# Optimization experiments

Measured on AMD Instinct MI355X. Metric: run time of the kernel, lower is better.

The kernel has to match this reference:

```python
import jax, jax.numpy as jnp
import numpy as np

N, E = 50000, 300000
NI, EI, H, OUT, L = 16, 8, 64, 3, 3  # node/edge input widths, hidden, output, conv_depth


def setup_inputs() -> dict:
    key = jax.random.key(0)
    ks = iter(jax.random.split(key, 64))
    def rn(shape, scale=0.05):
        return jax.random.normal(next(ks), shape, dtype=jnp.float32) * scale
    inp = {}
    inp["nodes"] = jax.random.normal(next(ks), (N, NI), dtype=jnp.float32)
    inp["edges"] = jax.random.normal(next(ks), (E, EI), dtype=jnp.float32)
    inp["edge_idx"] = jax.random.randint(next(ks), (E, 2), 0, N, dtype=jnp.int32)
    def mlp_params(prefix, din, lead=None):
        s = () if lead is None else (lead,)
        inp[prefix + "_W1"] = rn(s + (din, H))
        inp[prefix + "_b1"] = jnp.zeros(s + (H,), jnp.float32)
        inp[prefix + "_W2"] = rn(s + (H, H))
        inp[prefix + "_b2"] = jnp.zeros(s + (H,), jnp.float32)
        inp[prefix + "_g"] = jnp.ones(s + (H,), jnp.float32)
        inp[prefix + "_be"] = jnp.zeros(s + (H,), jnp.float32)
    mlp_params("ne", NI)            # node encoder
    mlp_params("ee", EI)            # edge encoder
    mlp_params("nm", 2 * H, lead=L)  # node messengers (stacked over conv_depth)
    mlp_params("em", 3 * H, lead=L)  # edge messengers
    inp["dec_W1"] = rn((H, H)); inp["dec_b1"] = jnp.zeros((H,), jnp.float32)
    inp["dec_W2"] = rn((H, OUT)); inp["dec_b2"] = jnp.zeros((OUT,), jnp.float32)
    return inp


def _lrelu(x):
    return jnp.where(x >= 0, x, 0.05 * x)


def _ln(x, g, b):
    m = jnp.mean(x, axis=-1, keepdims=True)
    v = jnp.mean((x - m) ** 2, axis=-1, keepdims=True)
    return (x - m) * jax.lax.rsqrt(v + 1e-5) * g + b


def _mlp(x, W1, b1, W2, b2, g, b):
    h = _lrelu(x @ W1 + b1)
    h = _lrelu(h @ W2 + b2)
    return _ln(h, g, b)


def reference(nodes, edges, edge_idx,
              ne_W1, ne_b1, ne_W2, ne_b2, ne_g, ne_be,
              ee_W1, ee_b1, ee_W2, ee_b2, ee_g, ee_be,
              nm_W1, nm_b1, nm_W2, nm_b2, nm_g, nm_be,
              em_W1, em_b1, em_W2, em_b2, em_g, em_be,
              dec_W1, dec_b1, dec_W2, dec_b2):
    n = _mlp(nodes, ne_W1, ne_b1, ne_W2, ne_b2, ne_g, ne_be)   # [N, H]
    e = _mlp(edges, ee_W1, ee_b1, ee_W2, ee_b2, ee_g, ee_be)   # [E, H]
    s, r = edge_idx[:, 0], edge_idx[:, 1]
    for i in range(L):
        e = e + _mlp(jnp.concatenate([e, n[s], n[r]], axis=1),
                     em_W1[i], em_b1[i], em_W2[i], em_b2[i], em_g[i], em_be[i])
        aggr = jax.ops.segment_sum(e, s, num_segments=n.shape[0])  # scatter_add onto senders
        n = n + _mlp(jnp.concatenate([n, aggr], axis=1),
                     nm_W1[i], nm_b1[i], nm_W2[i], nm_b2[i], nm_g[i], nm_be[i])
    h = _lrelu(n @ dec_W1 + dec_b1)
    return h @ dec_W2 + dec_b2  # [N, OUT]
```

## Files before the change

### kernel.cpp

```cpp
#include <hip/hip_runtime.h>

constexpr int BT = 256;

typedef __attribute__((ext_vector_type(8))) short short8v;
typedef __attribute__((ext_vector_type(4))) short short4v;
typedef __attribute__((ext_vector_type(4))) float f32x4;

__device__ __forceinline__ float lrelu(float x) { return x >= 0.f ? x : 0.05f * x; }

__device__ __forceinline__ unsigned short bf16_rne(float x) {
    unsigned u = __float_as_uint(x);
    u += 0x7FFFu + ((u >> 16) & 1u);
    return (unsigned short)(u >> 16);
}
__device__ __forceinline__ float bf16_to_f(unsigned short h) {
    return __uint_as_float(((unsigned)h) << 16);
}
__device__ __forceinline__ void split2(float x, unsigned short& hi, unsigned short& lo) {
    hi = bf16_rne(x);
    lo = bf16_rne(x - bf16_to_f(hi));
}


__device__ __forceinline__ void stageA64(const float* __restrict__ src, int row0, int nrows,
                                         short* __restrict__ A)
{
    for (int q = threadIdx.x; q < 1024; q += 256) {
        const int row = q >> 4;
        const int k0 = (q & 15) << 2;
        const int grow = row0 + row;
        float4 x = (grow < nrows) ? *reinterpret_cast<const float4*>(src + (long long)grow * 64 + k0)
                                  : make_float4(0.f, 0.f, 0.f, 0.f);
        unsigned short h0,h1,h2,h3,l0,l1,l2,l3;
        split2(x.x, h0, l0); split2(x.y, h1, l1); split2(x.z, h2, l2); split2(x.w, h3, l3);
        const int off = row * 64 + ((((k0 >> 3) ^ (row & 7))) << 3) + (k0 & 7);
        short4v hv; hv[0]=(short)h0; hv[1]=(short)h1; hv[2]=(short)h2; hv[3]=(short)h3;
        short4v lv; lv[0]=(short)l0; lv[1]=(short)l1; lv[2]=(short)l2; lv[3]=(short)l3;
        *reinterpret_cast<short4v*>(A + off) = hv;
        *reinterpret_cast<short4v*>(A + 4096 + off) = lv;
    }
}

__device__ __forceinline__ void gemm64(const short* __restrict__ A, const short* __restrict__ wf,
                                       int row, int g, int lane, f32x4* __restrict__ acc)
{
    #pragma unroll
    for (int s = 0; s < 2; ++s) {
        const int k8 = s * 4 + g;
        const int aoff = row * 64 + ((k8 ^ (row & 7)) << 3);
        const short8v a_hi = *reinterpret_cast<const short8v*>(A + aoff);
        const short8v a_lo = *reinterpret_cast<const short8v*>(A + 4096 + aoff);
        #pragma unroll
        for (int t = 0; t < 4; ++t) {
            const short8v b_hi = *reinterpret_cast<const short8v*>(wf + ((s*4+t)*2+0)*512 + lane*8);
            const short8v b_lo = *reinterpret_cast<const short8v*>(wf + ((s*4+t)*2+1)*512 + lane*8);
            acc[t] = __builtin_amdgcn_mfma_f32_16x16x32_bf16(a_hi, b_hi, acc[t], 0, 0, 0);
            acc[t] = __builtin_amdgcn_mfma_f32_16x16x32_bf16(a_lo, b_hi, acc[t], 0, 0, 0);
            acc[t] = __builtin_amdgcn_mfma_f32_16x16x32_bf16(a_hi, b_lo, acc[t], 0, 0, 0);
        }
    }
}

__global__ void k_prepw(const float* __restrict__ emW1, const float* __restrict__ emW2,
                        const float* __restrict__ nmW1, const float* __restrict__ nmW2,
                        const float* __restrict__ eeW2, const float* __restrict__ neW2,
                        const float* __restrict__ decW1,
                        short* __restrict__ wf)
{
    const int cid = blockIdx.x;
    const float* src;
    if (cid < 21) {
        const int layer = cid / 7, j = cid % 7;
        src =
            j == 0 ? emW1 + (size_t)layer * 12288 :
            j == 1 ? emW1 + (size_t)layer * 12288 + 4096 :
            j == 2 ? emW1 + (size_t)layer * 12288 + 8192 :
            j == 3 ? emW2 + (size_t)layer * 4096 :
            j == 4 ? nmW1 + (size_t)layer * 8192 :
            j == 5 ? nmW1 + (size_t)layer * 8192 + 4096 :
                     nmW2 + (size_t)layer * 4096;
    } else {
        src = (cid == 21) ? eeW2 : (cid == 22) ? neW2 : decW1;
    }
    short* dst = wf + (size_t)cid * 8192;
    for (int fr = threadIdx.x; fr < 1024; fr += 256) {
        const int lane = fr & 63;
        const int stp = fr >> 6;
        const int p = stp & 1;
        const int st = stp >> 1;
        const int s = st >> 2, t = st & 3;
        const int col = ((lane & 15) << 2) + t;
        const int k0 = s * 32 + (lane >> 4) * 8;
        short8v o;
        #pragma unroll
        for (int i = 0; i < 8; ++i) {
            const float w = src[(k0 + i) * 64 + col];
            const unsigned short hi = bf16_rne(w);
            o[i] = (short)(p ? bf16_rne(w - bf16_to_f(hi)) : hi);
        }
        *reinterpret_cast<short8v*>(dst + fr * 8) = o;
    }
}

template<int DIN, bool PERM>
__global__ __launch_bounds__(256) void k_enc_mf(
    const float* __restrict__ x, const int* __restrict__ csr,
    const float* __restrict__ W1, const float* __restrict__ b1,
    const short* __restrict__ wfW2, const float* __restrict__ b2,
    const float* __restrict__ gam, const float* __restrict__ bet,
    float* __restrict__ out, int nrows)
{
    __shared__ short Hf[8192];
    const int row0 = blockIdx.x * 64;
    const int lane = threadIdx.x & 63;
    const int wm = threadIdx.x >> 6;
    const int g = lane >> 4, c = lane & 15;
    const int c4 = c << 2;
    const int rowA = wm * 16 + c;

    long long orig[4];
    #pragma unroll
    for (int r = 0; r < 4; ++r) {
        const int grow = row0 + wm * 16 + g * 4 + r;
        orig[r] = (grow < nrows) ? (long long)(PERM ? csr[grow] : grow) : -1;
    }

    const f32x4 z4 = {0.f, 0.f, 0.f, 0.f};
    f32x4 acc[4];
    #pragma unroll
    for (int t = 0; t < 4; ++t) acc[t] = z4;

    #pragma unroll
    for (int kq = 0; kq < DIN / 4; ++kq) {
        float xv[4][4];
        #pragma unroll
        for (int r = 0; r < 4; ++r) {
            float4 t4 = make_float4(0.f, 0.f, 0.f, 0.f);
            if (orig[r] >= 0)
                t4 = *reinterpret_cast<const float4*>(x + orig[r] * DIN + kq * 4);
            xv[r][0] = t4.x; xv[r][1] = t4.y; xv[r][2] = t4.z; xv[r][3] = t4.w;
        }
        #pragma unroll
        for (int i = 0; i < 4; ++i) {
            const int k = kq * 4 + i;
            const float4 w4 = *reinterpret_cast<const float4*>(W1 + k * 64 + c4);
            const float wv[4] = {w4.x, w4.y, w4.z, w4.w};
            #pragma unroll
            for (int t = 0; t < 4; ++t)
                #pragma unroll
                for (int r = 0; r < 4; ++r)
                    acc[t][r] = fmaf(xv[r][i], wv[t], acc[t][r]);
        }
    }

    const float4 b1q = *reinterpret_cast<const float4*>(b1 + c4);
    const float b1a[4] = {b1q.x, b1q.y, b1q.z, b1q.w};
    #pragma unroll
    for (int r = 0; r < 4; ++r) {
        const int rl = wm * 16 + g * 4 + r;
        const int off = rl * 64 + (((c4 >> 3) ^ (rl & 7)) << 3) + (c4 & 7);
        short4v hv, lv;
        #pragma unroll
        for (int t = 0; t < 4; ++t) {
            const float h = lrelu(acc[t][r] + b1a[t]);
            unsigned short hi, lo; split2(h, hi, lo);
            hv[t] = (short)hi; lv[t] = (short)lo;
        }
        *reinterpret_cast<short4v*>(Hf + off) = hv;
        *reinterpret_cast<short4v*>(Hf + 4096 + off) = lv;
    }

    f32x4 acc2[4];
    #pragma unroll
    for (int t = 0; t < 4; ++t) acc2[t] = z4;
    gemm64(Hf, wfW2, rowA, g, lane, acc2);

    const float4 b2q = *reinterpret_cast<const float4*>(b2 + c4);
    const float b2a[4] = {b2q.x, b2q.y, b2q.z, b2q.w};
    #pragma unroll
    for (int t = 0; t < 4; ++t) {
        #pragma unroll
        for (int r = 0; r < 4; ++r) acc2[t][r] = lrelu(acc2[t][r] + b2a[t]);
    }
    const float4 gq = *reinterpret_cast<const float4*>(gam + c4);
    const float4 bq = *reinterpret_cast<const float4*>(bet + c4);
    const float gv[4] = {gq.x, gq.y, gq.z, gq.w};
    const float bv[4] = {bq.x, bq.y, bq.z, bq.w};
    #pragma unroll
    for (int r = 0; r < 4; ++r) {
        float s = acc2[0][r] + acc2[1][r] + acc2[2][r] + acc2[3][r];
        s += __shfl_xor(s, 1); s += __shfl_xor(s, 2); s += __shfl_xor(s, 4); s += __shfl_xor(s, 8);
        const float mu = s * 0.015625f;
        float q = 0.f;
        #pragma unroll
        for (int t = 0; t < 4; ++t) { const float d = acc2[t][r] - mu; q = fmaf(d, d, q); }
        q += __shfl_xor(q, 1); q += __shfl_xor(q, 2); q += __shfl_xor(q, 4); q += __shfl_xor(q, 8);
        const float rs = rsqrtf(q * 0.015625f + 1e-5f);
        const int grow = row0 + wm * 16 + g * 4 + r;
        if (grow < nrows) {
            float4 o;
            o.x = (acc2[0][r] - mu) * rs * gv[0] + bv[0];
            o.y = (acc2[1][r] - mu) * rs * gv[1] + bv[1];
            o.z = (acc2[2][r] - mu) * rs * gv[2] + bv[2];
            o.w = (acc2[3][r] - mu) * rs * gv[3] + bv[3];
            *reinterpret_cast<float4*>(out + (long long)grow * 64 + c4) = o;
        }
    }
}

__global__ __launch_bounds__(256) void k_uv_mf(
    const float* __restrict__ n, const short* __restrict__ wfB, const short* __restrict__ wfC,
    float* __restrict__ u, float* __restrict__ v, int N)
{
    __shared__ short Ab[8192];
    const int row0 = blockIdx.x * 64;
    stageA64(n, row0, N, Ab);
    __syncthreads();
    const int lane = threadIdx.x & 63;
    const int wm = threadIdx.x >> 6;
    const int g = lane >> 4, c = lane & 15;
    const int c4 = c << 2;
    const int rowA = wm * 16 + c;
    const f32x4 z4 = {0.f, 0.f, 0.f, 0.f};
    f32x4 acc[4];
    #pragma unroll
    for (int t = 0; t < 4; ++t) acc[t] = z4;
    gemm64(Ab, wfB, rowA, g, lane, acc);
    #pragma unroll
    for (int r = 0; r < 4; ++r) {
        const int grow = row0 + wm * 16 + g * 4 + r;
        if (grow < N) {
            float4 o; o.x = acc[0][r]; o.y = acc[1][r]; o.z = acc[2][r]; o.w = acc[3][r];
            *reinterpret_cast<float4*>(u + (long long)grow * 64 + c4) = o;
        }
    }
    #pragma unroll
    for (int t = 0; t < 4; ++t) acc[t] = z4;
    gemm64(Ab, wfC, rowA, g, lane, acc);
    #pragma unroll
    for (int r = 0; r < 4; ++r) {
        const int grow = row0 + wm * 16 + g * 4 + r;
        if (grow < N) {
            float4 o; o.x = acc[0][r]; o.y = acc[1][r]; o.z = acc[2][r]; o.w = acc[3][r];
            *reinterpret_cast<float4*>(v + (long long)grow * 64 + c4) = o;
        }
    }
}

__global__ __launch_bounds__(256, 4) void k_edge_mf(
    float* __restrict__ e, const int* __restrict__ sp, const int* __restrict__ rp,
    const float* __restrict__ u, const float* __restrict__ v,
    const short* __restrict__ wfA, const short* __restrict__ wfW2,
    const float* __restrict__ b1, const float* __restrict__ b2,
    const float* __restrict__ gam, const float* __restrict__ bet, int E)
{
    __shared__ short Ab[8192];
    const int row0 = blockIdx.x * 64;
    const int lane = threadIdx.x & 63;
    const int wm = threadIdx.x >> 6;
    const int g = lane >> 4, c = lane & 15;
    const int c4 = c << 2;
    const int rowA = wm * 16 + c;

    int sidx[4], ridx[4];
    #pragma unroll
    for (int r = 0; r < 4; ++r) {
        const int grow = row0 + wm * 16 + g * 4 + r;
        if (grow < E) { sidx[r] = sp[grow]; ridx[r] = rp[grow]; }
        else          { sidx[r] = 0; ridx[r] = 0; }
    }
    float4 uu[4], vv[4];
    #pragma unroll
    for (int r = 0; r < 4; ++r) {
        uu[r] = *reinterpret_cast<const float4*>(u + (long long)sidx[r] * 64 + c4);
        vv[r] = *reinterpret_cast<const float4*>(v + (long long)ridx[r] * 64 + c4);
    }

    stageA64(e, row0, E, Ab);
    __syncthreads();

    const f32x4 z4 = {0.f, 0.f, 0.f, 0.f};
    f32x4 acc[4];
    #pragma unroll
    for (int t = 0; t < 4; ++t) acc[t] = z4;
    gemm64(Ab, wfA, rowA, g, lane, acc);

    const float4 b1q = *reinterpret_cast<const float4*>(b1 + c4);
    #pragma unroll
    for (int r = 0; r < 4; ++r) {
        acc[0][r] += b1q.x + uu[r].x + vv[r].x;
        acc[1][r] += b1q.y + uu[r].y + vv[r].y;
        acc[2][r] += b1q.z + uu[r].z + vv[r].z;
        acc[3][r] += b1q.w + uu[r].w + vv[r].w;
    }
    short4v eh[4], el[4];
    #pragma unroll
    for (int r = 0; r < 4; ++r) {
        const int rl = wm * 16 + g * 4 + r;
        const int off = rl * 64 + (((c4 >> 3) ^ (rl & 7)) << 3) + (c4 & 7);
        eh[r] = *reinterpret_cast<const short4v*>(Ab + off);
        el[r] = *reinterpret_cast<const short4v*>(Ab + 4096 + off);
        short4v hv, lv;
        #pragma unroll
        for (int t = 0; t < 4; ++t) {
            const float h = lrelu(acc[t][r]);
            unsigned short hi, lo; split2(h, hi, lo);
            hv[t] = (short)hi; lv[t] = (short)lo;
        }
        *reinterpret_cast<short4v*>(Ab + off) = hv;
        *reinterpret_cast<short4v*>(Ab + 4096 + off) = lv;
    }
    f32x4 acc2[4];
    #pragma unroll
    for (int t = 0; t < 4; ++t) acc2[t] = z4;
    gemm64(Ab, wfW2, rowA, g, lane, acc2);

    const float4 b2q = *reinterpret_cast<const float4*>(b2 + c4);
    const float b2a[4] = {b2q.x, b2q.y, b2q.z, b2q.w};
    #pragma unroll
    for (int t = 0; t < 4; ++t) {
        #pragma unroll
        for (int r = 0; r < 4; ++r) acc2[t][r] = lrelu(acc2[t][r] + b2a[t]);
    }
    const float4 gq = *reinterpret_cast<const float4*>(gam + c4);
    const float4 bq = *reinterpret_cast<const float4*>(bet + c4);
    const float gv[4] = {gq.x, gq.y, gq.z, gq.w};
    const float bv[4] = {bq.x, bq.y, bq.z, bq.w};
    #pragma unroll
    for (int r = 0; r < 4; ++r) {
        float s = acc2[0][r] + acc2[1][r] + acc2[2][r] + acc2[3][r];
        s += __shfl_xor(s, 1); s += __shfl_xor(s, 2); s += __shfl_xor(s, 4); s += __shfl_xor(s, 8);
        const float mu = s * 0.015625f;
        float q = 0.f;
        #pragma unroll
        for (int t = 0; t < 4; ++t) { const float d = acc2[t][r] - mu; q = fmaf(d, d, q); }
        q += __shfl_xor(q, 1); q += __shfl_xor(q, 2); q += __shfl_xor(q, 4); q += __shfl_xor(q, 8);
        const float rs = rsqrtf(q * 0.015625f + 1e-5f);
        const int grow = row0 + wm * 16 + g * 4 + r;
        if (grow < E) {
            float4 o;
            o.x = (acc2[0][r] - mu) * rs * gv[0] + bv[0] + bf16_to_f((unsigned short)eh[r][0]) + bf16_to_f((unsigned short)el[r][0]);
            o.y = (acc2[1][r] - mu) * rs * gv[1] + bv[1] + bf16_to_f((unsigned short)eh[r][1]) + bf16_to_f((unsigned short)el[r][1]);
            o.z = (acc2[2][r] - mu) * rs * gv[2] + bv[2] + bf16_to_f((unsigned short)eh[r][2]) + bf16_to_f((unsigned short)el[r][2]);
            o.w = (acc2[3][r] - mu) * rs * gv[3] + bv[3] + bf16_to_f((unsigned short)eh[r][3]) + bf16_to_f((unsigned short)el[r][3]);
            *reinterpret_cast<float4*>(e + (long long)grow * 64 + c4) = o;
        }
    }
}

__global__ __launch_bounds__(256) void k_node_mf(
    float* __restrict__ n, const float* __restrict__ aggr,
    const short* __restrict__ wfW1a, const short* __restrict__ wfW1b, const short* __restrict__ wfW2,
    const float* __restrict__ b1, const float* __restrict__ b2,
    const float* __restrict__ gam, const float* __restrict__ bet, int N)
{
    __shared__ short An[8192];
    __shared__ short Aa[8192];
    const int row0 = blockIdx.x * 64;
    stageA64(n, row0, N, An);
    stageA64(aggr, row0, N, Aa);
    __syncthreads();
    const int lane = threadIdx.x & 63;
    const int wm = threadIdx.x >> 6;
    const int g = lane >> 4, c = lane & 15;
    const int c4 = c << 2;
    const int rowA = wm * 16 + c;
    const f32x4 z4 = {0.f, 0.f, 0.f, 0.f};
    f32x4 acc[4];
    #pragma unroll
    for (int t = 0; t < 4; ++t) acc[t] = z4;
    gemm64(An, wfW1a, rowA, g, lane, acc);
    gemm64(Aa, wfW1b, rowA, g, lane, acc);

    const float4 b1q = *reinterpret_cast<const float4*>(b1 + c4);
    const float b1a[4] = {b1q.x, b1q.y, b1q.z, b1q.w};
    #pragma unroll
    for (int r = 0; r < 4; ++r) {
        const int rl = wm * 16 + g * 4 + r;
        const int off = rl * 64 + (((c4 >> 3) ^ (rl & 7)) << 3) + (c4 & 7);
        short4v hv, lv;
        #pragma unroll
        for (int t = 0; t < 4; ++t) {
            const float h = lrelu(acc[t][r] + b1a[t]);
            unsigned short hi, lo; split2(h, hi, lo);
            hv[t] = (short)hi; lv[t] = (short)lo;
        }
        *reinterpret_cast<short4v*>(Aa + off) = hv;
        *reinterpret_cast<short4v*>(Aa + 4096 + off) = lv;
    }
    f32x4 acc2[4];
    #pragma unroll
    for (int t = 0; t < 4; ++t) acc2[t] = z4;
    gemm64(Aa, wfW2, rowA, g, lane, acc2);

    const float4 b2q = *reinterpret_cast<const float4*>(b2 + c4);
    const float b2a[4] = {b2q.x, b2q.y, b2q.z, b2q.w};
    #pragma unroll
    for (int t = 0; t < 4; ++t) {
        #pragma unroll
        for (int r = 0; r < 4; ++r) acc2[t][r] = lrelu(acc2[t][r] + b2a[t]);
    }
    const float4 gq = *reinterpret_cast<const float4*>(gam + c4);
    const float4 bq = *reinterpret_cast<const float4*>(bet + c4);
    const float gv[4] = {gq.x, gq.y, gq.z, gq.w};
    const float bv[4] = {bq.x, bq.y, bq.z, bq.w};
    #pragma unroll
    for (int r = 0; r < 4; ++r) {
        float s = acc2[0][r] + acc2[1][r] + acc2[2][r] + acc2[3][r];
        s += __shfl_xor(s, 1); s += __shfl_xor(s, 2); s += __shfl_xor(s, 4); s += __shfl_xor(s, 8);
        const float mu = s * 0.015625f;
        float q = 0.f;
        #pragma unroll
        for (int t = 0; t < 4; ++t) { const float d = acc2[t][r] - mu; q = fmaf(d, d, q); }
        q += __shfl_xor(q, 1); q += __shfl_xor(q, 2); q += __shfl_xor(q, 4); q += __shfl_xor(q, 8);
        const float rs = rsqrtf(q * 0.015625f + 1e-5f);
        const int rl = wm * 16 + g * 4 + r;
        const int grow = row0 + rl;
        if (grow < N) {
            const int off = rl * 64 + (((c4 >> 3) ^ (rl & 7)) << 3) + (c4 & 7);
            const short4v nh = *reinterpret_cast<const short4v*>(An + off);
            const short4v nl = *reinterpret_cast<const short4v*>(An + 4096 + off);
            float4 o;
            o.x = (acc2[0][r] - mu) * rs * gv[0] + bv[0] + bf16_to_f((unsigned short)nh[0]) + bf16_to_f((unsigned short)nl[0]);
            o.y = (acc2[1][r] - mu) * rs * gv[1] + bv[1] + bf16_to_f((unsigned short)nh[1]) + bf16_to_f((unsigned short)nl[1]);
            o.z = (acc2[2][r] - mu) * rs * gv[2] + bv[2] + bf16_to_f((unsigned short)nh[2]) + bf16_to_f((unsigned short)nl[2]);
            o.w = (acc2[3][r] - mu) * rs * gv[3] + bv[3] + bf16_to_f((unsigned short)nh[3]) + bf16_to_f((unsigned short)nl[3]);
            *reinterpret_cast<float4*>(n + (long long)grow * 64 + c4) = o;
        }
    }
}

__global__ __launch_bounds__(256) void k_dec_mf(
    const float* __restrict__ n, const short* __restrict__ wfW1, const float* __restrict__ b1,
    const float* __restrict__ W2, const float* __restrict__ b2,
    float* __restrict__ out, int N)
{
    __shared__ short An[8192];
    float* hrow = reinterpret_cast<float*>(An);
    const int row0 = blockIdx.x * 64;
    stageA64(n, row0, N, An);
    __syncthreads();
    const int lane = threadIdx.x & 63;
    const int wm = threadIdx.x >> 6;
    const int g = lane >> 4, c = lane & 15;
    const int c4 = c << 2;
    const int rowA = wm * 16 + c;
    const f32x4 z4 = {0.f, 0.f, 0.f, 0.f};
    f32x4 acc[4];
    #pragma unroll
    for (int t = 0; t < 4; ++t) acc[t] = z4;
    gemm64(An, wfW1, rowA, g, lane, acc);
    const float4 b1q = *reinterpret_cast<const float4*>(b1 + c4);
    const float b1a[4] = {b1q.x, b1q.y, b1q.z, b1q.w};
    __syncthreads();
    #pragma unroll
    for (int t = 0; t < 4; ++t) {
        const int col = c4 + t;
        #pragma unroll
        for (int r = 0; r < 4; ++r) {
            const int rl = wm * 16 + g * 4 + r;
            hrow[rl * 64 + (col ^ (rl & 31))] = lrelu(acc[t][r] + b1a[t]);
        }
    }
    __syncthreads();
    const int row = threadIdx.x >> 2, o = threadIdx.x & 3;
    if (o < 3 && row0 + row < N) {
        float s = b2[o];
        #pragma unroll 8
        for (int k = 0; k < 64; ++k)
            s = fmaf(hrow[row * 64 + (k ^ (row & 31))], W2[k * 3 + o], s);
        out[(long long)(row0 + row) * 3 + o] = s;
    }
}

__global__ void k_hist(const int* __restrict__ eidx, int* __restrict__ cnt, int E)
{
    int i = blockIdx.x * 256 + threadIdx.x;
    if (i < E) atomicAdd(&cnt[eidx[2 * i]], 1);
}

__global__ void k_scan1(const int* __restrict__ cnt, int* __restrict__ starts,
                        int* __restrict__ bsum, int n)
{
    __shared__ int sh[256];
    const int tid = threadIdx.x;
    const int i = blockIdx.x * 256 + tid;
    const int val = (i < n) ? cnt[i] : 0;
    sh[tid] = val; __syncthreads();
    for (int off = 1; off < 256; off <<= 1) {
        int t = (tid >= off) ? sh[tid - off] : 0;
        __syncthreads();
        sh[tid] += t;
        __syncthreads();
    }
    if (i < n) starts[i] = sh[tid] - val;
    if (tid == 255) bsum[blockIdx.x] = sh[255];
}

__global__ void k_scan2(int* __restrict__ bsum, int nb)
{
    __shared__ int sh[256];
    const int tid = threadIdx.x;
    const int val = (tid < nb) ? bsum[tid] : 0;
    sh[tid] = val; __syncthreads();
    for (int off = 1; off < 256; off <<= 1) {
        int t = (tid >= off) ? sh[tid - off] : 0;
        __syncthreads();
        sh[tid] += t;
        __syncthreads();
    }
    if (tid < nb) bsum[tid] = sh[tid] - val;
}

__global__ void k_scan3(int* __restrict__ starts, const int* __restrict__ bsum, int n)
{
    int i = blockIdx.x * 256 + threadIdx.x;
    if (i < n) starts[i] += bsum[blockIdx.x];
}

__global__ void k_scatter(const int* __restrict__ eidx, const int* __restrict__ starts,
                          int* __restrict__ cursor, int* __restrict__ csr,
                          int* __restrict__ sp, int* __restrict__ rp, int E)
{
    int i = blockIdx.x * 256 + threadIdx.x;
    if (i < E) {
        const int s = eidx[2 * i];
        const int p = atomicAdd(&cursor[s], 1);
        const int q = starts[s] + p;
        csr[q] = i;
        sp[q] = s;
        rp[q] = eidx[2 * i + 1];
    }
}

__global__ __launch_bounds__(256) void k_aggr(
    const float* __restrict__ e, const int* __restrict__ starts, const int* __restrict__ cnt,
    float* __restrict__ aggr, int N)
{
    const int node = blockIdx.x * 4 + (threadIdx.x >> 6);
    if (node >= N) return;
    const int j = threadIdx.x & 63;
    const int st = starts[node], en = st + cnt[node];
    float a = 0.f;
    for (int t = st; t < en; ++t)
        a += e[(long long)t * 64 + j];
    aggr[(long long)node * 64 + j] = a;
}

extern "C" void kernel_launch(void* const* d_in, const int* in_sizes, int n_in,
                              void* d_out, int out_size, void* d_ws, size_t ws_size,
                              hipStream_t stream)
{
    (void)in_sizes; (void)n_in; (void)out_size; (void)ws_size;
    constexpr int N = 50000, E = 300000, L = 3;

    const float* nodes = (const float*)d_in[0];
    const float* edges = (const float*)d_in[1];
    const int*   eidx  = (const int*)d_in[2];
    const float* neW1 = (const float*)d_in[3];
    const float* neb1 = (const float*)d_in[4];
    const float* neW2 = (const float*)d_in[5];
    const float* neb2 = (const float*)d_in[6];
    const float* neg  = (const float*)d_in[7];
    const float* nebe = (const float*)d_in[8];
    const float* eeW1 = (const float*)d_in[9];
    const float* eeb1 = (const float*)d_in[10];
    const float* eeW2 = (const float*)d_in[11];
    const float* eeb2 = (const float*)d_in[12];
    const float* eeg  = (const float*)d_in[13];
    const float* eebe = (const float*)d_in[14];
    const float* nmW1 = (const float*)d_in[15];
    const float* nmb1 = (const float*)d_in[16];
    const float* nmW2 = (const float*)d_in[17];
    const float* nmb2 = (const float*)d_in[18];
    const float* nmg  = (const float*)d_in[19];
    const float* nmbe = (const float*)d_in[20];
    const float* emW1 = (const float*)d_in[21];
    const float* emb1 = (const float*)d_in[22];
    const float* emW2 = (const float*)d_in[23];
    const float* emb2 = (const float*)d_in[24];
    const float* emg  = (const float*)d_in[25];
    const float* embe = (const float*)d_in[26];
    const float* decW1 = (const float*)d_in[27];
    const float* decb1 = (const float*)d_in[28];
    const float* decW2 = (const float*)d_in[29];
    const float* decb2 = (const float*)d_in[30];

    float* n   = (float*)d_ws;
    float* u   = n + (size_t)N * 64;
    float* v   = u + (size_t)N * 64;
    float* e   = v + (size_t)N * 64;
    int* cnt    = (int*)(e + (size_t)E * 64);
    int* starts = cnt + N;
    int* csr    = starts + N;
    int* bsum   = csr + E;
    int* cursor = bsum + 256;
    int* sp     = cursor + N;
    int* rp     = sp + E;
    short* wf   = (short*)(rp + E);

    const int nbN = (N + BT - 1) / BT;
    const int nbE = (E + BT - 1) / BT;
    const int nbN64 = (N + 63) / 64;
    const int nbE64 = (E + 63) / 64;

    const short* wfEE  = wf + (size_t)21 * 8192;
    const short* wfNE  = wf + (size_t)22 * 8192;
    const short* wfDec = wf + (size_t)23 * 8192;

    k_prepw<<<24, 256, 0, stream>>>(emW1, emW2, nmW1, nmW2, eeW2, neW2, decW1, wf);
    hipMemsetAsync(cnt, 0, (size_t)N * sizeof(int), stream);
    hipMemsetAsync(cursor, 0, (size_t)N * sizeof(int), stream);
    k_hist<<<nbE, 256, 0, stream>>>(eidx, cnt, E);
    k_scan1<<<nbN, 256, 0, stream>>>(cnt, starts, bsum, N);
    k_scan2<<<1, 256, 0, stream>>>(bsum, nbN);
    k_scan3<<<nbN, 256, 0, stream>>>(starts, bsum, N);
    k_scatter<<<nbE, 256, 0, stream>>>(eidx, starts, cursor, csr, sp, rp, E);

    k_enc_mf<16, false><<<nbN64, 256, 0, stream>>>(nodes, nullptr, neW1, neb1, wfNE,
                                                   neb2, neg, nebe, n, N);
    k_enc_mf<8, true><<<nbE64, 256, 0, stream>>>(edges, csr, eeW1, eeb1, wfEE,
                                                 eeb2, eeg, eebe, e, E);

    for (int i = 0; i < L; ++i) {
        const short* wl = wf + (size_t)i * 7 * 8192;
        k_uv_mf<<<nbN64, 256, 0, stream>>>(n, wl + 8192, wl + 2 * 8192, u, v, N);
        k_edge_mf<<<nbE64, 256, 0, stream>>>(e, sp, rp, u, v, wl, wl + 3 * 8192,
                                             emb1 + i * 64, emb2 + i * 64,
                                             emg + i * 64, embe + i * 64, E);
        k_aggr<<<(N + 3) / 4, 256, 0, stream>>>(e, starts, cnt, u, N);
        k_node_mf<<<nbN64, 256, 0, stream>>>(n, u, wl + 4 * 8192, wl + 5 * 8192, wl + 6 * 8192,
                                             nmb1 + i * 64, nmb2 + i * 64,
                                             nmg + i * 64, nmbe + i * 64, N);
    }
    k_dec_mf<<<nbN64, 256, 0, stream>>>(n, wfDec, decb1, decW2, decb2, (float*)d_out, N);
}
```

Baseline: 472.8 us.

## Fuse u/v projection and segment aggregation into node kernels, use wave-local staging

Removes the separate k_uv_mf and k_aggr kernels. The next layer's u/v projections are now computed inside the node-encoder and node-update kernels, and the CSR segment sum is computed inside the node kernel. Shared-memory staging is made per-wave, so block-wide __syncthreads become wave barriers, and occupancy hints are raised. The decoder's second layer now uses shuffle reductions instead of an LDS round trip. This cuts launches and global round trips for u, v and aggr, but the node kernel now does a serial, load-imbalanced gather per wave over 16 nodes.

New measurement: 489.8 us. 3.6% more time.

```diff
diff --git a/kernel.cpp b/kernel.cpp
--- a/kernel.cpp
+++ b/kernel.cpp
@@ -1,6 +1,4 @@
 #include <hip/hip_runtime.h>
-
-constexpr int BT = 256;
 
 typedef __attribute__((ext_vector_type(8))) short short8v;
 typedef __attribute__((ext_vector_type(4))) short short4v;
@@ -22,18 +20,20 @@
 }
 
 
-__device__ __forceinline__ void stageA64(const float* __restrict__ src, int row0, int nrows,
-                                         short* __restrict__ A)
-{
-    for (int q = threadIdx.x; q < 1024; q += 256) {
-        const int row = q >> 4;
+__device__ __forceinline__ void stageW(const float* __restrict__ src, int row0, int nrows,
+                                       short* __restrict__ A, int wm, int lane)
+{
+    #pragma unroll
+    for (int it = 0; it < 4; ++it) {
+        const int q = it * 64 + lane;
+        const int rl = wm * 16 + (q >> 4);
         const int k0 = (q & 15) << 2;
-        const int grow = row0 + row;
+        const int grow = row0 + rl;
         float4 x = (grow < nrows) ? *reinterpret_cast<const float4*>(src + (long long)grow * 64 + k0)
                                   : make_float4(0.f, 0.f, 0.f, 0.f);
         unsigned short h0,h1,h2,h3,l0,l1,l2,l3;
         split2(x.x, h0, l0); split2(x.y, h1, l1); split2(x.z, h2, l2); split2(x.w, h3, l3);
-        const int off = row * 64 + ((((k0 >> 3) ^ (row & 7))) << 3) + (k0 & 7);
+        const int off = rl * 64 + ((((k0 >> 3) ^ (rl & 7))) << 3) + (k0 & 7);
         short4v hv; hv[0]=(short)h0; hv[1]=(short)h1; hv[2]=(short)h2; hv[3]=(short)h3;
         short4v lv; lv[0]=(short)l0; lv[1]=(short)l1; lv[2]=(short)l2; lv[3]=(short)l3;
         *reinterpret_cast<short4v*>(A + off) = hv;
@@ -58,6 +58,22 @@
             acc[t] = __builtin_amdgcn_mfma_f32_16x16x32_bf16(a_lo, b_hi, acc[t], 0, 0, 0);
             acc[t] = __builtin_amdgcn_mfma_f32_16x16x32_bf16(a_hi, b_lo, acc[t], 0, 0, 0);
         }
+    }
+}
+
+__device__ __forceinline__ void repackW(short* __restrict__ A, const float4* __restrict__ q,
+                                        int wm, int g, int c4)
+{
+    #pragma unroll
+    for (int r = 0; r < 4; ++r) {
+        const int rl = wm * 16 + g * 4 + r;
+        const int off = rl * 64 + (((c4 >> 3) ^ (rl & 7)) << 3) + (c4 & 7);
+        unsigned short h0,h1,h2,h3,l0,l1,l2,l3;
+        split2(q[r].x, h0, l0); split2(q[r].y, h1, l1); split2(q[r].z, h2, l2); split2(q[r].w, h3, l3);
+        short4v hv; hv[0]=(short)h0; hv[1]=(short)h1; hv[2]=(short)h2; hv[3]=(short)h3;
+        short4v lv; lv[0]=(short)l0; lv[1]=(short)l1; lv[2]=(short)l2; lv[3]=(short)l3;
+        *reinterpret_cast<short4v*>(A + off) = hv;
+        *reinterpret_cast<short4v*>(A + 4096 + off) = lv;
     }
 }
 
@@ -102,13 +118,15 @@
     }
 }
 
-template<int DIN, bool PERM>
-__global__ __launch_bounds__(256) void k_enc_mf(
+template<int DIN, bool PERM, bool MAKEUV>
+__global__ __launch_bounds__(256, 4) void k_enc_mf(
     const float* __restrict__ x, const int* __restrict__ csr,
     const float* __restrict__ W1, const float* __restrict__ b1,
     const short* __restrict__ wfW2, const float* __restrict__ b2,
     const float* __restrict__ gam, const float* __restrict__ bet,
-    float* __restrict__ out, int nrows)
+    float* __restrict__ out,
+    const short* __restrict__ wfB, const short* __restrict__ wfC,
+    float* __restrict__ u, float* __restrict__ v, int nrows)
 {
     __shared__ short Hf[8192];
     const int row0 = blockIdx.x * 64;
@@ -154,21 +172,16 @@
     }
 
     const float4 b1q = *reinterpret_cast<const float4*>(b1 + c4);
-    const float b1a[4] = {b1q.x, b1q.y, b1q.z, b1q.w};
-    #pragma unroll
-    for (int r = 0; r < 4; ++r) {
-        const int rl = wm * 16 + g * 4 + r;
-        const int off = rl * 64 + (((c4 >> 3) ^ (rl & 7)) << 3) + (c4 & 7);
-        short4v hv, lv;
-        #pragma unroll
-        for (int t = 0; t < 4; ++t) {
-            const float h = lrelu(acc[t][r] + b1a[t]);
-            unsigned short hi, lo; split2(h, hi, lo);
-            hv[t] = (short)hi; lv[t] = (short)lo;
-        }
-        *reinterpret_cast<short4v*>(Hf + off) = hv;
-        *reinterpret_cast<short4v*>(Hf + 4096 + off) = lv;
-    }
+    float4 hq[4];
+    #pragma unroll
+    for (int r = 0; r < 4; ++r) {
+        hq[r].x = lrelu(acc[0][r] + b1q.x);
+        hq[r].y = lrelu(acc[1][r] + b1q.y);
+        hq[r].z = lrelu(acc[2][r] + b1q.z);
+        hq[r].w = lrelu(acc[3][r] + b1q.w);
+    }
+    repackW(Hf, hq, wm, g, c4);
+    __builtin_amdgcn_wave_barrier();
 
     f32x4 acc2[4];
     #pragma unroll
@@ -184,8 +197,7 @@
     }
     const float4 gq = *reinterpret_cast<const float4*>(gam + c4);
     const float4 bq = *reinterpret_cast<const float4*>(bet + c4);
-    const float gv[4] = {gq.x, gq.y, gq.z, gq.w};
-    const float bv[4] = {bq.x, bq.y, bq.z, bq.w};
+    float4 nq[4];
     #pragma unroll
     for (int r = 0; r < 4; ++r) {
         float s = acc2[0][r] + acc2[1][r] + acc2[2][r] + acc2[3][r];
@@ -196,58 +208,44 @@
         for (int t = 0; t < 4; ++t) { const float d = acc2[t][r] - mu; q = fmaf(d, d, q); }
         q += __shfl_xor(q, 1); q += __shfl_xor(q, 2); q += __shfl_xor(q, 4); q += __shfl_xor(q, 8);
         const float rs = rsqrtf(q * 0.015625f + 1e-5f);
+        nq[r].x = (acc2[0][r] - mu) * rs * gq.x + bq.x;
+        nq[r].y = (acc2[1][r] - mu) * rs * gq.y + bq.y;
+        nq[r].z = (acc2[2][r] - mu) * rs * gq.z + bq.z;
+        nq[r].w = (acc2[3][r] - mu) * rs * gq.w + bq.w;
         const int grow = row0 + wm * 16 + g * 4 + r;
-        if (grow < nrows) {
-            float4 o;
-            o.x = (acc2[0][r] - mu) * rs * gv[0] + bv[0];
-            o.y = (acc2[1][r] - mu) * rs * gv[1] + bv[1];
-            o.z = (acc2[2][r] - mu) * rs * gv[2] + bv[2];
-            o.w = (acc2[3][r] - mu) * rs * gv[3] + bv[3];
-            *reinterpret_cast<float4*>(out + (long long)grow * 64 + c4) = o;
-        }
-    }
-}
-
-__global__ __launch_bounds__(256) void k_uv_mf(
-    const float* __restrict__ n, const short* __restrict__ wfB, const short* __restrict__ wfC,
-    float* __restrict__ u, float* __restrict__ v, int N)
-{
-    __shared__ short Ab[8192];
-    const int row0 = blockIdx.x * 64;
-    stageA64(n, row0, N, Ab);
-    __syncthreads();
-    const int lane = threadIdx.x & 63;
-    const int wm = threadIdx.x >> 6;
-    const int g = lane >> 4, c = lane & 15;
-    const int c4 = c << 2;
-    const int rowA = wm * 16 + c;
-    const f32x4 z4 = {0.f, 0.f, 0.f, 0.f};
-    f32x4 acc[4];
-    #pragma unroll
-    for (int t = 0; t < 4; ++t) acc[t] = z4;
-    gemm64(Ab, wfB, rowA, g, lane, acc);
-    #pragma unroll
-    for (int r = 0; r < 4; ++r) {
-        const int grow = row0 + wm * 16 + g * 4 + r;
-        if (grow < N) {
-            float4 o; o.x = acc[0][r]; o.y = acc[1][r]; o.z = acc[2][r]; o.w = acc[3][r];
-            *reinterpret_cast<float4*>(u + (long long)grow * 64 + c4) = o;
-        }
-    }
-    #pragma unroll
-    for (int t = 0; t < 4; ++t) acc[t] = z4;
-    gemm64(Ab, wfC, rowA, g, lane, acc);
-    #pragma unroll
-    for (int r = 0; r < 4; ++r) {
-        const int grow = row0 + wm * 16 + g * 4 + r;
-        if (grow < N) {
-            float4 o; o.x = acc[0][r]; o.y = acc[1][r]; o.z = acc[2][r]; o.w = acc[3][r];
-            *reinterpret_cast<float4*>(v + (long long)grow * 64 + c4) = o;
-        }
-    }
-}
-
-__global__ __launch_bounds__(256, 4) void k_edge_mf(
+        if (grow < nrows)
+            *reinterpret_cast<float4*>(out + (long long)grow * 64 + c4) = nq[r];
+    }
+
+    if (MAKEUV) {
+        repackW(Hf, nq, wm, g, c4);
+        __builtin_amdgcn_wave_barrier();
+        #pragma unroll
+        for (int t = 0; t < 4; ++t) acc2[t] = z4;
+        gemm64(Hf, wfB, rowA, g, lane, acc2);
+        #pragma unroll
+        for (int r = 0; r < 4; ++r) {
+            const int grow = row0 + wm * 16 + g * 4 + r;
+            if (grow < nrows) {
+                float4 o; o.x = acc2[0][r]; o.y = acc2[1][r]; o.z = acc2[2][r]; o.w = acc2[3][r];
+                *reinterpret_cast<float4*>(u + (long long)grow * 64 + c4) = o;
+            }
+        }
+        #pragma unroll
+        for (int t = 0; t < 4; ++t) acc2[t] = z4;
+        gemm64(Hf, wfC, rowA, g, lane, acc2);
+        #pragma unroll
+        for (int r = 0; r < 4; ++r) {
+            const int grow = row0 + wm * 16 + g * 4 + r;
+            if (grow < nrows) {
+                float4 o; o.x = acc2[0][r]; o.y = acc2[1][r]; o.z = acc2[2][r]; o.w = acc2[3][r];
+                *reinterpret_cast<float4*>(v + (long long)grow * 64 + c4) = o;
+            }
+        }
+    }
+}
+
+__global__ __launch_bounds__(256, 6) void k_edge_mf(
     float* __restrict__ e, const int* __restrict__ sp, const int* __restrict__ rp,
     const float* __restrict__ u, const float* __restrict__ v,
     const short* __restrict__ wfA, const short* __restrict__ wfW2,
@@ -269,6 +267,8 @@
         if (grow < E) { sidx[r] = sp[grow]; ridx[r] = rp[grow]; }
         else          { sidx[r] = 0; ridx[r] = 0; }
     }
+    stageW(e, row0, E, Ab, wm, lane);
+    __builtin_amdgcn_wave_barrier();
     float4 uu[4], vv[4];
     #pragma unroll
     for (int r = 0; r < 4; ++r) {
@@ -276,9 +276,6 @@
         vv[r] = *reinterpret_cast<const float4*>(v + (long long)ridx[r] * 64 + c4);
     }
 
-    stageA64(e, row0, E, Ab);
-    __syncthreads();
-
     const f32x4 z4 = {0.f, 0.f, 0.f, 0.f};
     f32x4 acc[4];
     #pragma unroll
@@ -286,12 +283,13 @@
     gemm64(Ab, wfA, rowA, g, lane, acc);
 
     const float4 b1q = *reinterpret_cast<const float4*>(b1 + c4);
-    #pragma unroll
-    for (int r = 0; r < 4; ++r) {
-        acc[0][r] += b1q.x + uu[r].x + vv[r].x;
-        acc[1][r] += b1q.y + uu[r].y + vv[r].y;
-        acc[2][r] += b1q.z + uu[r].z + vv[r].z;
-        acc[3][r] += b1q.w + uu[r].w + vv[r].w;
+    float4 hq[4];
+    #pragma unroll
+    for (int r = 0; r < 4; ++r) {
+        hq[r].x = lrelu(acc[0][r] + b1q.x + uu[r].x + vv[r].x);
+        hq[r].y = lrelu(acc[1][r] + b1q.y + uu[r].y + vv[r].y);
+        hq[r].z = lrelu(acc[2][r] + b1q.z + uu[r].z + vv[r].z);
+        hq[r].w = lrelu(acc[3][r] + b1q.w + uu[r].w + vv[r].w);
     }
     short4v eh[4], el[4];
     #pragma unroll
@@ -300,16 +298,11 @@
         const int off = rl * 64 + (((c4 >> 3) ^ (rl & 7)) << 3) + (c4 & 7);
         eh[r] = *reinterpret_cast<const short4v*>(Ab + off);
         el[r] = *reinterpret_cast<const short4v*>(Ab + 4096 + off);
-        short4v hv, lv;
-        #pragma unroll
-        for (int t = 0; t < 4; ++t) {
-            const float h = lrelu(acc[t][r]);
-            unsigned short hi, lo; split2(h, hi, lo);
-            hv[t] = (short)hi; lv[t] = (short)lo;
-        }
-        *reinterpret_cast<short4v*>(Ab + off) = hv;
-        *reinterpret_cast<short4v*>(Ab + 4096 + off) = lv;
-    }
+    }
+    __builtin_amdgcn_wave_barrier();
+    repackW(Ab, hq, wm, g, c4);
+    __builtin_amdgcn_wave_barrier();
+
     f32x4 acc2[4];
     #pragma unroll
     for (int t = 0; t < 4; ++t) acc2[t] = z4;
@@ -324,8 +317,6 @@
     }
     const float4 gq = *reinterpret_cast<const float4*>(gam + c4);
     const float4 bq = *reinterpret_cast<const float4*>(bet + c4);
-    const float gv[4] = {gq.x, gq.y, gq.z, gq.w};
-    const float bv[4] = {bq.x, bq.y, bq.z, bq.w};
     #pragma unroll
     for (int r = 0; r < 4; ++r) {
         float s = acc2[0][r] + acc2[1][r] + acc2[2][r] + acc2[3][r];
@@ -339,32 +330,54 @@
         const int grow = row0 + wm * 16 + g * 4 + r;
         if (grow < E) {
             float4 o;
-            o.x = (acc2[0][r] - mu) * rs * gv[0] + bv[0] + bf16_to_f((unsigned short)eh[r][0]) + bf16_to_f((unsigned short)el[r][0]);
-            o.y = (acc2[1][r] - mu) * rs * gv[1] + bv[1] + bf16_to_f((unsigned short)eh[r][1]) + bf16_to_f((unsigned short)el[r][1]);
-            o.z = (acc2[2][r] - mu) * rs * gv[2] + bv[2] + bf16_to_f((unsigned short)eh[r][2]) + bf16_to_f((unsigned short)el[r][2]);
-            o.w = (acc2[3][r] - mu) * rs * gv[3] + bv[3] + bf16_to_f((unsigned short)eh[r][3]) + bf16_to_f((unsigned short)el[r][3]);
+            o.x = (acc2[0][r] - mu) * rs * gq.x + bq.x + bf16_to_f((unsigned short)eh[r][0]) + bf16_to_f((unsigned short)el[r][0]);
+            o.y = (acc2[1][r] - mu) * rs * gq.y + bq.y + bf16_to_f((unsigned short)eh[r][1]) + bf16_to_f((unsigned short)el[r][1]);
+            o.z = (acc2[2][r] - mu) * rs * gq.z + bq.z + bf16_to_f((unsigned short)eh[r][2]) + bf16_to_f((unsigned short)el[r][2]);
+            o.w = (acc2[3][r] - mu) * rs * gq.w + bq.w + bf16_to_f((unsigned short)eh[r][3]) + bf16_to_f((unsigned short)el[r][3]);
             *reinterpret_cast<float4*>(e + (long long)grow * 64 + c4) = o;
         }
     }
 }
 
-__global__ __launch_bounds__(256) void k_node_mf(
-    float* __restrict__ n, const float* __restrict__ aggr,
+__global__ __launch_bounds__(256, 4) void k_node_mf(
+    float* __restrict__ n, const float* __restrict__ e,
+    const int* __restrict__ starts, const int* __restrict__ cnt,
     const short* __restrict__ wfW1a, const short* __restrict__ wfW1b, const short* __restrict__ wfW2,
     const float* __restrict__ b1, const float* __restrict__ b2,
-    const float* __restrict__ gam, const float* __restrict__ bet, int N)
+    const float* __restrict__ gam, const float* __restrict__ bet,
+    const short* __restrict__ wfB, const short* __restrict__ wfC,
+    float* __restrict__ u, float* __restrict__ v, int N)
 {
     __shared__ short An[8192];
     __shared__ short Aa[8192];
     const int row0 = blockIdx.x * 64;
-    stageA64(n, row0, N, An);
-    stageA64(aggr, row0, N, Aa);
-    __syncthreads();
     const int lane = threadIdx.x & 63;
     const int wm = threadIdx.x >> 6;
     const int g = lane >> 4, c = lane & 15;
     const int c4 = c << 2;
     const int rowA = wm * 16 + c;
+
+    stageW(n, row0, N, An, wm, lane);
+
+    const int n0 = row0 + wm * 16;
+    #pragma unroll 1
+    for (int li = 0; li < 16; ++li) {
+        const int node = n0 + li;
+        float a = 0.f;
+        if (node < N) {
+            const int st = starts[node];
+            const int en = st + cnt[node];
+            for (int t = st; t < en; ++t)
+                a += e[(long long)t * 64 + lane];
+        }
+        unsigned short hi, lo; split2(a, hi, lo);
+        const int rl = wm * 16 + li;
+        const int off = rl * 64 + (((lane >> 3) ^ (rl & 7)) << 3) + (lane & 7);
+        Aa[off] = (short)hi;
+        Aa[4096 + off] = (short)lo;
+    }
+    __builtin_amdgcn_wave_barrier();
+
     const f32x4 z4 = {0.f, 0.f, 0.f, 0.f};
     f32x4 acc[4];
     #pragma unroll
@@ -373,21 +386,18 @@
     gemm64(Aa, wfW1b, rowA, g, lane, acc);
 
     const float4 b1q = *reinterpret_cast<const float4*>(b1 + c4);
-    const float b1a[4] = {b1q.x, b1q.y, b1q.z, b1q.w};
-    #pragma unroll
-    for (int r = 0; r < 4; ++r) {
-        const int rl = wm * 16 + g * 4 + r;
-        const int off = rl * 64 + (((c4 >> 3) ^ (rl & 7)) << 3) + (c4 & 7);
-        short4v hv, lv;
-        #pragma unroll
-        for (int t = 0; t < 4; ++t) {
-            const float h = lrelu(acc[t][r] + b1a[t]);
-            unsigned short hi, lo; split2(h, hi, lo);
-            hv[t] = (short)hi; lv[t] = (short)lo;
-        }
-        *reinterpret_cast<short4v*>(Aa + off) = hv;
-        *reinterpret_cast<short4v*>(Aa + 4096 + off) = lv;
-    }
+    float4 hq[4];
+    #pragma unroll
+    for (int r = 0; r < 4; ++r) {
+        hq[r].x = lrelu(acc[0][r] + b1q.x);
+        hq[r].y = lrelu(acc[1][r] + b1q.y);
+        hq[r].z = lrelu(acc[2][r] + b1q.z);
+        hq[r].w = lrelu(acc[3][r] + b1q.w);
+    }
+    __builtin_amdgcn_wave_barrier();
+    repackW(Aa, hq, wm, g, c4);
+    __builtin_amdgcn_wave_barrier();
+
     f32x4 acc2[4];
     #pragma unroll
     for (int t = 0; t < 4; ++t) acc2[t] = z4;
@@ -402,8 +412,7 @@
     }
     const float4 gq = *reinterpret_cast<const float4*>(gam + c4);
     const float4 bq = *reinterpret_cast<const float4*>(bet + c4);
-    const float gv[4] = {gq.x, gq.y, gq.z, gq.w};
-    const float bv[4] = {bq.x, bq.y, bq.z, bq.w};
+    float4 nq[4];
     #pragma unroll
     for (int r = 0; r < 4; ++r) {
         float s = acc2[0][r] + acc2[1][r] + acc2[2][r] + acc2[3][r];
@@ -415,36 +424,61 @@
         q += __shfl_xor(q, 1); q += __shfl_xor(q, 2); q += __shfl_xor(q, 4); q += __shfl_xor(q, 8);
         const float rs = rsqrtf(q * 0.015625f + 1e-5f);
         const int rl = wm * 16 + g * 4 + r;
+        const int off = rl * 64 + (((c4 >> 3) ^ (rl & 7)) << 3) + (c4 & 7);
+        const short4v nh = *reinterpret_cast<const short4v*>(An + off);
+        const short4v nl = *reinterpret_cast<const short4v*>(An + 4096 + off);
+        nq[r].x = (acc2[0][r] - mu) * rs * gq.x + bq.x + bf16_to_f((unsigned short)nh[0]) + bf16_to_f((unsigned short)nl[0]);
+        nq[r].y = (acc2[1][r] - mu) * rs * gq.y + bq.y + bf16_to_f((unsigned short)nh[1]) + bf16_to_f((unsigned short)nl[1]);
+        nq[r].z = (acc2[2][r] - mu) * rs * gq.z + bq.z + bf16_to_f((unsigned short)nh[2]) + bf16_to_f((unsigned short)nl[2]);
+        nq[r].w = (acc2[3][r] - mu) * rs * gq.w + bq.w + bf16_to_f((unsigned short)nh[3]) + bf16_to_f((unsigned short)nl[3]);
         const int grow = row0 + rl;
-        if (grow < N) {
-            const int off = rl * 64 + (((c4 >> 3) ^ (rl & 7)) << 3) + (c4 & 7);
-            const short4v nh = *reinterpret_cast<const short4v*>(An + off);
-            const short4v nl = *reinterpret_cast<const short4v*>(An + 4096 + off);
-            float4 o;
-            o.x = (acc2[0][r] - mu) * rs * gv[0] + bv[0] + bf16_to_f((unsigned short)nh[0]) + bf16_to_f((unsigned short)nl[0]);
-            o.y = (acc2[1][r] - mu) * rs * gv[1] + bv[1] + bf16_to_f((unsigned short)nh[1]) + bf16_to_f((unsigned short)nl[1]);
-            o.z = (acc2[2][r] - mu) * rs * gv[2] + bv[2] + bf16_to_f((unsigned short)nh[2]) + bf16_to_f((unsigned short)nl[2]);
-            o.w = (acc2[3][r] - mu) * rs * gv[3] + bv[3] + bf16_to_f((unsigned short)nh[3]) + bf16_to_f((unsigned short)nl[3]);
-            *reinterpret_cast<float4*>(n + (long long)grow * 64 + c4) = o;
-        }
-    }
-}
-
-__global__ __launch_bounds__(256) void k_dec_mf(
+        if (grow < N)
+            *reinterpret_cast<float4*>(n + (long long)grow * 64 + c4) = nq[r];
+    }
+
+    if (wfB) {
+        __builtin_amdgcn_wave_barrier();
+        repackW(An, nq, wm, g, c4);
+        __builtin_amdgcn_wave_barrier();
+        #pragma unroll
+        for (int t = 0; t < 4; ++t) acc2[t] = z4;
+        gemm64(An, wfB, rowA, g, lane, acc2);
+        #pragma unroll
+        for (int r = 0; r < 4; ++r) {
+            const int grow = row0 + wm * 16 + g * 4 + r;
+            if (grow < N) {
+                float4 o; o.x = acc2[0][r]; o.y = acc2[1][r]; o.z = acc2[2][r]; o.w = acc2[3][r];
+                *reinterpret_cast<float4*>(u + (long long)grow * 64 + c4) = o;
+            }
+        }
+        #pragma unroll
+        for (int t = 0; t < 4; ++t) acc2[t] = z4;
+        gemm64(An, wfC, rowA, g, lane, acc2);
+        #pragma unroll
+        for (int r = 0; r < 4; ++r) {
+            const int grow = row0 + wm * 16 + g * 4 + r;
+            if (grow < N) {
+                float4 o; o.x = acc2[0][r]; o.y = acc2[1][r]; o.z = acc2[2][r]; o.w = acc2[3][r];
+                *reinterpret_cast<float4*>(v + (long long)grow * 64 + c4) = o;
+            }
+        }
+    }
+}
+
+__global__ __launch_bounds__(256, 4) void k_dec_mf(
     const float* __restrict__ n, const short* __restrict__ wfW1, const float* __restrict__ b1,
     const float* __restrict__ W2, const float* __restrict__ b2,
     float* __restrict__ out, int N)
 {
     __shared__ short An[8192];
-    float* hrow = reinterpret_cast<float*>(An);
     const int row0 = blockIdx.x * 64;
-    stageA64(n, row0, N, An);
-    __syncthreads();
     const int lane = threadIdx.x & 63;
     const int wm = threadIdx.x >> 6;
     const int g = lane >> 4, c = lane & 15;
     const int c4 = c << 2;
     const int rowA = wm * 16 + c;
+    stageW(n, row0, N, An, wm, lane);
+    __builtin_amdgcn_wave_barrier();
     const f32x4 z4 = {0.f, 0.f, 0.f, 0.f};
     f32x4 acc[4];
     #pragma unroll
@@ -452,24 +486,34 @@
     gemm64(An, wfW1, rowA, g, lane, acc);
     const float4 b1q = *reinterpret_cast<const float4*>(b1 + c4);
     const float b1a[4] = {b1q.x, b1q.y, b1q.z, b1q.w};
-    __syncthreads();
-    #pragma unroll
-    for (int t = 0; t < 4; ++t) {
-        const int col = c4 + t;
+    #pragma unroll
+    for (int t = 0; t < 4; ++t)
+        #pragma unroll
+        for (int r = 0; r < 4; ++r) acc[t][r] = lrelu(acc[t][r] + b1a[t]);
+    const float4 w0 = *reinterpret_cast<const float4*>(W2 + c4 * 3);
+    const float4 w1 = *reinterpret_cast<const float4*>(W2 + c4 * 3 + 4);
+    const float4 w2 = *reinterpret_cast<const float4*>(W2 + c4 * 3 + 8);
+    const float wv[12] = {w0.x,w0.y,w0.z,w0.w, w1.x,w1.y,w1.z,w1.w, w2.x,w2.y,w2.z,w2.w};
+    float po[4][3];
+    #pragma unroll
+    for (int r = 0; r < 4; ++r)
+        #pragma unroll
+        for (int o = 0; o < 3; ++o)
+            po[r][o] = acc[0][r]*wv[o] + acc[1][r]*wv[3+o] + acc[2][r]*wv[6+o] + acc[3][r]*wv[9+o];
+    #pragma unroll
+    for (int m = 1; m <= 8; m <<= 1)
+        #pragma unroll
+        for (int r = 0; r < 4; ++r)
+            #pragma unroll
+            for (int o = 0; o < 3; ++o)
+                po[r][o] += __shfl_xor(po[r][o], m);
+    if (c < 3) {
         #pragma unroll
         for (int r = 0; r < 4; ++r) {
-            const int rl = wm * 16 + g * 4 + r;
-            hrow[rl * 64 + (col ^ (rl & 31))] = lrelu(acc[t][r] + b1a[t]);
-        }
-    }
-    __syncthreads();
-    const int row = threadIdx.x >> 2, o = threadIdx.x & 3;
-    if (o < 3 && row0 + row < N) {
-        float s = b2[o];
-        #pragma unroll 8
-        for (int k = 0; k < 64; ++k)
-            s = fmaf(hrow[row * 64 + (k ^ (row & 31))], W2[k * 3 + o], s);
-        out[(long long)(row0 + row) * 3 + o] = s;
+            const int grow = row0 + wm * 16 + g * 4 + r;
+            const float val = (c == 0) ? po[r][0] : (c == 1) ? po[r][1] : po[r][2];
+            if (grow < N) out[(long long)grow * 3 + c] = b2[c] + val;
+        }
     }
 }
 
@@ -531,20 +575,6 @@
         sp[q] = s;
         rp[q] = eidx[2 * i + 1];
     }
-}
-
-__global__ __launch_bounds__(256) void k_aggr(
-    const float* __restrict__ e, const int* __restrict__ starts, const int* __restrict__ cnt,
-    float* __restrict__ aggr, int N)
-{
-    const int node = blockIdx.x * 4 + (threadIdx.x >> 6);
-    if (node >= N) return;
-    const int j = threadIdx.x & 63;
-    const int st = starts[node], en = st + cnt[node];
-    float a = 0.f;
-    for (int t = st; t < en; ++t)
-        a += e[(long long)t * 64 + j];
-    aggr[(long long)node * 64 + j] = a;
 }
 
 extern "C" void kernel_launch(void* const* d_in, const int* in_sizes, int n_in,
@@ -599,8 +629,8 @@
     int* rp     = sp + E;
     short* wf   = (short*)(rp + E);
 
-    const int nbN = (N + BT - 1) / BT;
-    const int nbE = (E + BT - 1) / BT;
+    const int nbN = (N + 255) / 256;
+    const int nbE = (E + 255) / 256;
     const int nbN64 = (N + 63) / 64;
     const int nbE64 = (E + 63) / 64;
 
@@ -617,21 +647,27 @@
     k_scan3<<<nbN, 256, 0, stream>>>(starts, bsum, N);
     k_scatter<<<nbE, 256, 0, stream>>>(eidx, starts, cursor, csr, sp, rp, E);
 
-    k_enc_mf<16, false><<<nbN64, 256, 0, stream>>>(nodes, nullptr, neW1, neb1, wfNE,
-                                                   neb2, neg, nebe, n, N);
-    k_enc_mf<8, true><<<nbE64, 256, 0, stream>>>(edges, csr, eeW1, eeb1, wfEE,
-                                                 eeb2, eeg, eebe, e, E);
+    const short* wl0 = wf;
+    k_enc_mf<16, false, true><<<nbN64, 256, 0, stream>>>(
+        nodes, nullptr, neW1, neb1, wfNE, neb2, neg, nebe, n,
+        wl0 + 8192, wl0 + 2 * 8192, u, v, N);
+    k_enc_mf<8, true, false><<<nbE64, 256, 0, stream>>>(
+        edges, csr, eeW1, eeb1, wfEE, eeb2, eeg, eebe, e,
+        nullptr, nullptr, nullptr, nullptr, E);
 
     for (int i = 0; i < L; ++i) {
         const short* wl = wf + (size_t)i * 7 * 8192;
-        k_uv_mf<<<nbN64, 256, 0, stream>>>(n, wl + 8192, wl + 2 * 8192, u, v, N);
         k_edge_mf<<<nbE64, 256, 0, stream>>>(e, sp, rp, u, v, wl, wl + 3 * 8192,
                                              emb1 + i * 64, emb2 + i * 64,
                                              emg + i * 64, embe + i * 64, E);
-        k_aggr<<<(N + 3) / 4, 256, 0, stream>>>(e, starts, cnt, u, N);
-        k_node_mf<<<nbN64, 256, 0, stream>>>(n, u, wl + 4 * 8192, wl + 5 * 8192, wl + 6 * 8192,
+        const short* wln = (i + 1 < L) ? wf + (size_t)(i + 1) * 7 * 8192 : nullptr;
+        k_node_mf<<<nbN64, 256, 0, stream>>>(n, e, starts, cnt,
+                                             wl + 4 * 8192, wl + 5 * 8192, wl + 6 * 8192,
                                              nmb1 + i * 64, nmb2 + i * 64,
-                                             nmg + i * 64, nmbe + i * 64, N);
+                                             nmg + i * 64, nmbe + i * 64,
+                                             wln ? wln + 8192 : nullptr,
+                                             wln ? wln + 2 * 8192 : nullptr,
+                                             u, v, N);
     }
     k_dec_mf<<<nbN64, 256, 0, stream>>>(n, wfDec, decb1, decW2, decb2, (float*)d_out, N);
 }
```
